# Kernel tuning notes

Measured on AMD Instinct MI355X. Metric: run time of the kernel, lower is better.

Reference implementation:

```python
import jax, jax.numpy as jnp
import numpy as np

NUM_HEADS = 16
HEAD_DIM = 64
D_DEC = 1024
D_ENC = 1024
R = 256  # kv_lora_rank
LN_EPS = 1e-5


def setup_inputs() -> dict:
    key = jax.random.key(0)
    ks = jax.random.split(key, 8)
    B, SQ, SK = 4, 2048, 4096
    query = jax.random.normal(ks[0], (B, SQ, D_DEC), dtype=jnp.float32)
    encoder_output = jax.random.normal(ks[1], (B, SK, D_ENC), dtype=jnp.float32)
    s = 0.02
    Wq = jax.random.normal(ks[2], (NUM_HEADS * HEAD_DIM, D_DEC), dtype=jnp.float32) * s
    Wkva = jax.random.normal(ks[3], (R, D_ENC), dtype=jnp.float32) * s
    ln_g = jnp.ones((R,), dtype=jnp.float32)
    ln_b = jnp.zeros((R,), dtype=jnp.float32)
    Wkvb = jax.random.normal(ks[4], (NUM_HEADS * 2 * HEAD_DIM, R), dtype=jnp.float32) * s
    Wout = jax.random.normal(ks[5], (D_DEC, NUM_HEADS * HEAD_DIM), dtype=jnp.float32) * s
    return {"query": query, "encoder_output": encoder_output, "Wq": Wq,
            "Wkva": Wkva, "ln_g": ln_g, "ln_b": ln_b, "Wkvb": Wkvb, "Wout": Wout}


def reference(query, encoder_output, Wq, Wkva, ln_g, ln_b, Wkvb, Wout):
    B, SQ, _ = query.shape
    SK = encoder_output.shape[1]
    H, Dh = NUM_HEADS, HEAD_DIM

    # q projection -> [B, H, SQ, Dh]
    q = jnp.einsum('bsd,ed->bse', query, Wq).reshape(B, SQ, H, Dh).transpose(0, 2, 1, 3)

    # low-rank KV compression + layernorm
    c = jnp.einsum('bsd,rd->bsr', encoder_output, Wkva)  # [B, SK, R]
    mu = jnp.mean(c, axis=-1, keepdims=True)
    var = jnp.mean(jnp.square(c - mu), axis=-1, keepdims=True)
    c = (c - mu) * jax.lax.rsqrt(var + LN_EPS) * ln_g + ln_b

    # decompress to K,V: [B, SK, H, 2*Dh] -> split
    kv = jnp.einsum('bsr,er->bse', c, Wkvb).reshape(B, SK, H, 2 * Dh).transpose(0, 2, 1, 3)
    k, v = kv[..., :Dh], kv[..., Dh:]

    scale = 1.0 / np.sqrt(Dh).astype(np.float32)
    scores = jnp.einsum('bhqd,bhkd->bhqk', q, k) * scale
    attn = jax.nn.softmax(scores, axis=-1)  # dropout is identity in eval / p=0
    o = jnp.einsum('bhqk,bhkd->bhqd', attn, v)
    o = o.transpose(0, 2, 1, 3).reshape(B, SQ, H * Dh)
    return jnp.einsum('bse,de->bsd', o, Wout)
```

## Files before the change

### kernel.cpp

```cpp
#include <hip/hip_runtime.h>

#define LOG2E 1.4426950408889634f

typedef __attribute__((ext_vector_type(8))) short short8;
typedef __attribute__((ext_vector_type(4))) float f32x4;
typedef __attribute__((ext_vector_type(16))) float f32x16;
typedef __attribute__((ext_vector_type(4))) unsigned u32x4;

__device__ inline unsigned short f2bf(float f) {
  unsigned u = __float_as_uint(f);
  u += 0x7fffu + ((u >> 16) & 1u);
  return (unsigned short)(u >> 16);
}

#define MFMA16(a, b, c) __builtin_amdgcn_mfma_f32_16x16x32_bf16((a), (b), (c), 0, 0, 0)
#define MFMA32(a, b, c) __builtin_amdgcn_mfma_f32_32x32x16_bf16((a), (b), (c), 0, 0, 0)

#define GLDS16(gp, lp)                                                              \
  __builtin_amdgcn_global_load_lds((const __attribute__((address_space(1))) void*)(gp), \
                                   (__attribute__((address_space(3))) void*)(lp), 16, 0, 0)

__device__ inline f32x4 zero4() {
  f32x4 z = {0.f, 0.f, 0.f, 0.f};
  return z;
}
__device__ inline f32x16 zero16() {
  f32x16 z = {0.f, 0.f, 0.f, 0.f, 0.f, 0.f, 0.f, 0.f, 0.f, 0.f, 0.f, 0.f, 0.f, 0.f, 0.f, 0.f};
  return z;
}
__device__ inline unsigned cvtpk_bf16(float a, float b) {
  unsigned r;
  asm("v_cvt_pk_bf16_f32 %0, %1, %2" : "=v"(r) : "v"(a), "v"(b));
  return r;
}
__device__ inline void plswap(unsigned& a, unsigned& b) {
  asm("v_permlane32_swap_b32 %0, %1" : "+v"(a), "+v"(b));
}

__global__ __launch_bounds__(256) void k_cast5(
    const float* __restrict__ q, const float* __restrict__ wq, const float* __restrict__ wo,
    const float* __restrict__ wb, const float* __restrict__ wa,
    unsigned short* __restrict__ qo, unsigned short* __restrict__ wqo, unsigned short* __restrict__ woo,
    unsigned short* __restrict__ wbo, unsigned short* __restrict__ wao) {
  int i = (blockIdx.x * 256 + threadIdx.x) * 4;
  const float* src;
  unsigned short* dst;
  int off;
  if (i < 8388608) { src = q; dst = qo; off = i; }
  else if (i < 9437184) { src = wq; dst = wqo; off = i - 8388608; }
  else if (i < 10485760) { src = wo; dst = woo; off = i - 9437184; }
  else if (i < 11010048) { src = wb; dst = wbo; off = i - 10485760; }
  else { src = wa; dst = wao; off = i - 11010048; }
  float4 v = *(const float4*)(src + off);
  unsigned lo = (unsigned)f2bf(v.x) | ((unsigned)f2bf(v.y) << 16);
  unsigned hi = (unsigned)f2bf(v.z) | ((unsigned)f2bf(v.w) << 16);
  *(uint2*)(dst + off) = make_uint2(lo, hi);
}

__global__ __launch_bounds__(256, 2) void k_qproj(const unsigned short* __restrict__ A,
                                                  const unsigned short* __restrict__ Bw,
                                                  unsigned short* __restrict__ Qout) {
  __shared__ __align__(16) short As[128 * 32];
  __shared__ __align__(16) short Bs[128 * 32];
  const int K = 1024;
  int tid = threadIdx.x;
  int w = tid >> 6, lane = tid & 63, quad = lane >> 4, c = lane & 15;
  int m0 = blockIdx.x * 128, n0 = blockIdx.y * 128;
  int wm = (w >> 1) * 64, wn = (w & 1) * 64;
  f32x4 acc[4][4];
#pragma unroll
  for (int i = 0; i < 4; i++)
#pragma unroll
    for (int j = 0; j < 4; j++) acc[i][j] = zero4();

  for (int k0 = 0; k0 < K; k0 += 32) {
#pragma unroll
    for (int i = 0; i < 2; i++) {
      int seg = w * 2 + i;
      int bo = seg * 1024 + lane * 16;
      int row = bo >> 6, col = (bo & 63) >> 1;
      GLDS16(A + (size_t)(m0 + row) * K + k0 + col, (char*)As + seg * 1024);
      GLDS16(Bw + (size_t)(n0 + row) * K + k0 + col, (char*)Bs + seg * 1024);
    }
    __syncthreads();
    short8 af[4], bfr[4];
#pragma unroll
    for (int i = 0; i < 4; i++) {
      af[i] = *(const short8*)&As[(wm + i * 16 + c) * 32 + quad * 8];
      bfr[i] = *(const short8*)&Bs[(wn + i * 16 + c) * 32 + quad * 8];
    }
#pragma unroll
    for (int mi = 0; mi < 4; mi++)
#pragma unroll
      for (int ni = 0; ni < 4; ni++) acc[mi][ni] = MFMA16(af[mi], bfr[ni], acc[mi][ni]);
    __syncthreads();
  }
  const float scale = 0.125f * LOG2E;
#pragma unroll
  for (int mi = 0; mi < 4; mi++) {
    int rowb = m0 + wm + mi * 16 + quad * 4;
#pragma unroll
    for (int ni = 0; ni < 4; ni++) {
      int col = n0 + wn + ni * 16 + c;
      int h = col >> 6, d = col & 63;
#pragma unroll
      for (int r = 0; r < 4; r++) {
        int row = rowb + r;
        int b = row >> 11, sq = row & 2047;
        Qout[(((size_t)(b * 16 + h)) * 2048 + sq) * 64 + d] = f2bf(acc[mi][ni][r] * scale);
      }
    }
  }
}

__global__ __launch_bounds__(256, 2) void k_cln(const float* __restrict__ E,
                                                const unsigned short* __restrict__ Wa,
                                                const float* __restrict__ g, const float* __restrict__ bb,
                                                unsigned short* __restrict__ Cout) {
  __shared__ __align__(16) short As[64 * 32];
  __shared__ __align__(16) short Bs[256 * 32];
  __shared__ float redS[4][64], redQ[4][64];
  __shared__ float gS[256], bS[256];
  const int K = 1024;
  int tid = threadIdx.x;
  int w = tid >> 6, lane = tid & 63, quad = lane >> 4, c = lane & 15;
  int m0 = blockIdx.x * 64;
  int rsub = lane >> 2, csub = (lane & 3) * 8;
  gS[tid] = g[tid];
  bS[tid] = bb[tid];
  f32x4 acc[4][4];
#pragma unroll
  for (int i = 0; i < 4; i++)
#pragma unroll
    for (int j = 0; j < 4; j++) acc[i][j] = zero4();

  for (int k0 = 0; k0 < K; k0 += 32) {
    {
      const float* Ep = E + (size_t)(m0 + w * 16 + rsub) * K + k0 + csub;
      float4 va = *(const float4*)Ep;
      float4 vb2 = *(const float4*)(Ep + 4);
      u32x4 pk = {cvtpk_bf16(va.x, va.y), cvtpk_bf16(va.z, va.w),
                  cvtpk_bf16(vb2.x, vb2.y), cvtpk_bf16(vb2.z, vb2.w)};
      *(u32x4*)((char*)As + w * 1024 + lane * 16) = pk;
    }
#pragma unroll
    for (int i = 0; i < 4; i++) {
      int seg = w * 4 + i;
      int bo = seg * 1024 + lane * 16;
      int row = bo >> 6, col = (bo & 63) >> 1;
      GLDS16(Wa + (size_t)row * K + k0 + col, (char*)Bs + seg * 1024);
    }
    __syncthreads();
    short8 af[4], bfr[4];
#pragma unroll
    for (int i = 0; i < 4; i++) {
      af[i] = *(const short8*)&As[(i * 16 + c) * 32 + quad * 8];
      bfr[i] = *(const short8*)&Bs[(w * 64 + i * 16 + c) * 32 + quad * 8];
    }
#pragma unroll
    for (int mi = 0; mi < 4; mi++)
#pragma unroll
      for (int ni = 0; ni < 4; ni++) acc[mi][ni] = MFMA16(af[mi], bfr[ni], acc[mi][ni]);
    __syncthreads();
  }
  float ps[4][4], pq[4][4];
#pragma unroll
  for (int mi = 0; mi < 4; mi++)
#pragma unroll
    for (int r = 0; r < 4; r++) {
      float s = 0.f, q = 0.f;
#pragma unroll
      for (int ni = 0; ni < 4; ni++) {
        float x = acc[mi][ni][r];
        s += x;
        q += x * x;
      }
      for (int m = 1; m < 16; m <<= 1) {
        s += __shfl_xor(s, m, 64);
        q += __shfl_xor(q, m, 64);
      }
      ps[mi][r] = s;
      pq[mi][r] = q;
    }
  if (c == 0) {
#pragma unroll
    for (int mi = 0; mi < 4; mi++)
#pragma unroll
      for (int r = 0; r < 4; r++) {
        int row = mi * 16 + quad * 4 + r;
        redS[w][row] = ps[mi][r];
        redQ[w][row] = pq[mi][r];
      }
  }
  __syncthreads();
  float muv[4][4], rsv[4][4];
#pragma unroll
  for (int mi = 0; mi < 4; mi++)
#pragma unroll
    for (int r = 0; r < 4; r++) {
      int row = mi * 16 + quad * 4 + r;
      float S = redS[0][row] + redS[1][row] + redS[2][row] + redS[3][row];
      float Q = redQ[0][row] + redQ[1][row] + redQ[2][row] + redQ[3][row];
      float mu = S * (1.f / 256.f);
      float var = Q * (1.f / 256.f) - mu * mu;
      muv[mi][r] = mu;
      rsv[mi][r] = rsqrtf(var + 1e-5f);
    }
#pragma unroll
  for (int mi = 0; mi < 4; mi++)
#pragma unroll
    for (int ni = 0; ni < 4; ni++) {
      int col = w * 64 + ni * 16 + c;
#pragma unroll
      for (int r = 0; r < 4; r++) {
        int row = m0 + mi * 16 + quad * 4 + r;
        float y = (acc[mi][ni][r] - muv[mi][r]) * rsv[mi][r] * gS[col] + bS[col];
        Cout[(size_t)row * 256 + col] = f2bf(y);
      }
    }
}

__global__ __launch_bounds__(256, 2) void k_kv(const unsigned short* __restrict__ A,
                                               const unsigned short* __restrict__ Bw,
                                               unsigned short* __restrict__ Kb,
                                               unsigned short* __restrict__ Vb) {
  __shared__ __align__(16) short As[128 * 32];
  __shared__ __align__(16) short Bs[128 * 32];
  const int K = 256;
  int tid = threadIdx.x;
  int w = tid >> 6, lane = tid & 63, quad = lane >> 4, c = lane & 15;
  int m0 = blockIdx.x * 128, n0 = blockIdx.y * 128;
  int wm = (w >> 1) * 64, wn = (w & 1) * 64;
  f32x4 acc[4][4];
#pragma unroll
  for (int i = 0; i < 4; i++)
#pragma unroll
    for (int j = 0; j < 4; j++) acc[i][j] = zero4();

  for (int k0 = 0; k0 < K; k0 += 32) {
#pragma unroll
    for (int i = 0; i < 2; i++) {
      int seg = w * 2 + i;
      int bo = seg * 1024 + lane * 16;
      int row = bo >> 6, col = (bo & 63) >> 1;
      GLDS16(A + (size_t)(m0 + row) * K + k0 + col, (char*)As + seg * 1024);
      GLDS16(Bw + (size_t)(n0 + row) * K + k0 + col, (char*)Bs + seg * 1024);
    }
    __syncthreads();
    short8 af[4], bfr[4];
#pragma unroll
    for (int i = 0; i < 4; i++) {
      af[i] = *(const short8*)&As[(wm + i * 16 + c) * 32 + quad * 8];
      bfr[i] = *(const short8*)&Bs[(wn + i * 16 + c) * 32 + quad * 8];
    }
#pragma unroll
    for (int mi = 0; mi < 4; mi++)
#pragma unroll
      for (int ni = 0; ni < 4; ni++) acc[mi][ni] = MFMA16(af[mi], bfr[ni], acc[mi][ni]);
    __syncthreads();
  }
#pragma unroll
  for (int mi = 0; mi < 4; mi++) {
    int rowb = m0 + wm + mi * 16 + quad * 4;
    int b = rowb >> 12;
    int sk0 = rowb & 4095;
    int kt = sk0 >> 6, ki0 = sk0 & 63;
    int sg = ((wm + mi * 16) & 63) >> 4;
    int khi = quad >> 1;
    int j0 = (quad & 1) * 4;
#pragma unroll
    for (int ni = 0; ni < 4; ni++) {
      int col = n0 + wn + ni * 16 + c;
      int h = col >> 7, rr = col & 127;
      size_t base = ((size_t)(b * 16 + h)) * 262144 + (size_t)kt * 4096;
      if (rr < 64) {
        int d = rr;
        int ds = d >> 4, dhi = (d >> 3) & 1, j = d & 7;
#pragma unroll
        for (int r = 0; r < 4; r++) {
          int ki = ki0 + r;
          int half = ki >> 5, l31k = ki & 31;
          Kb[base + (size_t)((half * 4 + ds) * 64 + l31k + 32 * dhi) * 8 + j] = f2bf(acc[mi][ni][r]);
        }
      } else {
        int d = rr - 64;
        int dt = d >> 5;
        unsigned lo = (unsigned)f2bf(acc[mi][ni][0]) | ((unsigned)f2bf(acc[mi][ni][1]) << 16);
        unsigned hi = (unsigned)f2bf(acc[mi][ni][2]) | ((unsigned)f2bf(acc[mi][ni][3]) << 16);
        *(uint2*)(Vb + base + (size_t)((dt * 4 + sg) * 64 + (d & 31) + 32 * khi) * 8 + j0) =
            make_uint2(lo, hi);
      }
    }
  }
}

__device__ __forceinline__ void attn_tile(const char* Kl, const char* Vl,
                                          const short8 (&qf)[4], f32x16 (&O)[2], float& lp) {
#pragma unroll
  for (int h = 0; h < 2; h++) {
    short8 kf[4];
#pragma unroll
    for (int ds = 0; ds < 4; ds++) kf[ds] = *(const short8*)(Kl + (h * 4 + ds) * 1024);
    f32x16 S = zero16();
#pragma unroll
    for (int ds = 0; ds < 4; ds++) S = MFMA32(kf[ds], qf[ds], S);
    float lpa = 0.f, lpb = 0.f;
    unsigned u[8];
#pragma unroll
    for (int m = 0; m < 8; m++) {
      float p0 = __builtin_amdgcn_exp2f(S[2 * m]);
      float p1 = __builtin_amdgcn_exp2f(S[2 * m + 1]);
      if (m & 1) lpb += p0 + p1; else lpa += p0 + p1;
      u[m] = cvtpk_bf16(p0, p1);
    }
    lp += lpa + lpb;
    plswap(u[0], u[2]);
    plswap(u[1], u[3]);
    plswap(u[4], u[6]);
    plswap(u[5], u[7]);
    u32x4 w0 = {u[0], u[1], u[2], u[3]};
    u32x4 w1 = {u[4], u[5], u[6], u[7]};
    short8 paf0 = __builtin_bit_cast(short8, w0);
    short8 paf1 = __builtin_bit_cast(short8, w1);
#pragma unroll
    for (int dt = 0; dt < 2; dt++) {
      short8 vf0 = *(const short8*)(Vl + (dt * 4 + h * 2 + 0) * 1024);
      short8 vf1 = *(const short8*)(Vl + (dt * 4 + h * 2 + 1) * 1024);
      O[dt] = MFMA32(paf0, vf0, O[dt]);
      O[dt] = MFMA32(paf1, vf1, O[dt]);
    }
  }
}

__global__ __launch_bounds__(256, 4) void k_attn(const unsigned short* __restrict__ Qb,
                                                 const unsigned short* __restrict__ Kb,
                                                 const unsigned short* __restrict__ Vb,
                                                 unsigned short* __restrict__ Ob) {
  __shared__ __align__(16) short KA[8192];
  __shared__ __align__(16) short KB[8192];
  int tid = threadIdx.x;
  int w = tid >> 6, lane = tid & 63;
  int l31 = lane & 31, hi = lane >> 5;
  int qt = blockIdx.x, bh = blockIdx.y;

  const char* Kg = (const char*)Kb + (size_t)bh * 524288;
  const char* Vg = (const char*)Vb + (size_t)bh * 524288;
  int ldsseg = (w < 2) ? w * 4 : 8 + (w - 2) * 4;
  const char* sgbase = ((w < 2) ? Kg + (w * 4) * 1024 : Vg + ((w - 2) * 4) * 1024) + lane * 16;

  const unsigned short* Qrow = Qb + ((size_t)bh * 2048 + qt * 128 + w * 32 + l31) * 64 + hi * 8;
  short8 qf[4];
#pragma unroll
  for (int ds = 0; ds < 4; ds++) qf[ds] = *(const short8*)(Qrow + ds * 16);

  f32x16 O[2];
  float lp = 0.f;
#pragma unroll
  for (int j = 0; j < 2; j++) O[j] = zero16();

#pragma unroll
  for (int i = 0; i < 4; i++) GLDS16(sgbase + i * 1024, (char*)KA + (ldsseg + i) * 1024);
  sgbase += 8192;
  __syncthreads();

  for (int kt2 = 0; kt2 < 64; kt2 += 2) {
    {
#pragma unroll
      for (int i = 0; i < 4; i++)
        GLDS16(sgbase + i * 1024, (char*)KB + (ldsseg + i) * 1024);
      sgbase += 8192;
      attn_tile((const char*)KA + lane * 16, (const char*)KA + lane * 16 + 8192, qf, O, lp);
      __syncthreads();
    }
    {
      if (kt2 < 62) {
#pragma unroll
        for (int i = 0; i < 4; i++)
          GLDS16(sgbase + i * 1024, (char*)KA + (ldsseg + i) * 1024);
        sgbase += 8192;
      }
      attn_tile((const char*)KB + lane * 16, (const char*)KB + lane * 16 + 8192, qf, O, lp);
      __syncthreads();
    }
  }

  lp += __shfl_xor(lp, 32, 64);
  int b = bh >> 4, hh = bh & 15;
#pragma unroll
  for (int r = 0; r < 16; r++) {
    int qrow = (r & 3) + 8 * (r >> 2) + 4 * hi;
    float inv = __builtin_amdgcn_rcpf(__shfl(lp, qrow, 64));
    size_t orow = ((size_t)b * 2048 + qt * 128 + w * 32 + qrow) * 1024 + hh * 64 + l31;
    Ob[orow] = f2bf(O[0][r] * inv);
    Ob[orow + 32] = f2bf(O[1][r] * inv);
  }
}

__global__ __launch_bounds__(256, 2) void k_out(const unsigned short* __restrict__ A,
                                                const unsigned short* __restrict__ Bw,
                                                float* __restrict__ Out) {
  __shared__ __align__(16) short As[128 * 32];
  __shared__ __align__(16) short Bs[128 * 32];
  const int K = 1024;
  int tid = threadIdx.x;
  int w = tid >> 6, lane = tid & 63, quad = lane >> 4, c = lane & 15;
  int m0 = blockIdx.x * 128, n0 = blockIdx.y * 128;
  int wm = (w >> 1) * 64, wn = (w & 1) * 64;
  f32x4 acc[4][4];
#pragma unroll
  for (int i = 0; i < 4; i++)
#pragma unroll
    for (int j = 0; j < 4; j++) acc[i][j] = zero4();

  for (int k0 = 0; k0 < K; k0 += 32) {
#pragma unroll
    for (int i = 0; i < 2; i++) {
      int seg = w * 2 + i;
      int bo = seg * 1024 + lane * 16;
      int row = bo >> 6, col = (bo & 63) >> 1;
      GLDS16(A + (size_t)(m0 + row) * K + k0 + col, (char*)As + seg * 1024);
      GLDS16(Bw + (size_t)(n0 + row) * K + k0 + col, (char*)Bs + seg * 1024);
    }
    __syncthreads();
    short8 af[4], bfr[4];
#pragma unroll
    for (int i = 0; i < 4; i++) {
      af[i] = *(const short8*)&As[(wm + i * 16 + c) * 32 + quad * 8];
      bfr[i] = *(const short8*)&Bs[(wn + i * 16 + c) * 32 + quad * 8];
    }
#pragma unroll
    for (int mi = 0; mi < 4; mi++)
#pragma unroll
      for (int ni = 0; ni < 4; ni++) acc[mi][ni] = MFMA16(af[mi], bfr[ni], acc[mi][ni]);
    __syncthreads();
  }
#pragma unroll
  for (int mi = 0; mi < 4; mi++) {
    int rowb = m0 + wm + mi * 16 + quad * 4;
#pragma unroll
    for (int ni = 0; ni < 4; ni++) {
      int col = n0 + wn + ni * 16 + c;
#pragma unroll
      for (int r = 0; r < 4; r++) Out[(size_t)(rowb + r) * 1024 + col] = acc[mi][ni][r];
    }
  }
}

extern "C" void kernel_launch(void* const* d_in, const int* in_sizes, int n_in,
                              void* d_out, int out_size, void* d_ws, size_t ws_size,
                              hipStream_t stream) {
  const float* query = (const float*)d_in[0];
  const float* enc = (const float*)d_in[1];
  const float* Wq = (const float*)d_in[2];
  const float* Wkva = (const float*)d_in[3];
  const float* ln_g = (const float*)d_in[4];
  const float* ln_b = (const float*)d_in[5];
  const float* Wkvb = (const float*)d_in[6];
  const float* Wout = (const float*)d_in[7];
  if (ws_size < 81264640) return;

  char* ws = (char*)d_ws;
  unsigned short* wq_bf = (unsigned short*)(ws + 0);
  unsigned short* wa_bf = (unsigned short*)(ws + 2097152);
  unsigned short* wb_bf = (unsigned short*)(ws + 2621440);
  unsigned short* wo_bf = (unsigned short*)(ws + 3670016);
  unsigned short* qproj = (unsigned short*)(ws + 5767168);
  unsigned short* cln = (unsigned short*)(ws + 22544384);
  unsigned short* vbuf = (unsigned short*)(ws + 30932992);
  unsigned short* qin_o = (unsigned short*)(ws + 64487424);
  unsigned short* kbuf = (unsigned short*)d_out;

  k_cast5<<<11008, 256, 0, stream>>>(query, Wq, Wout, Wkvb, Wkva,
                                     qin_o, wq_bf, wo_bf, wb_bf, wa_bf);

  k_qproj<<<dim3(64, 8), 256, 0, stream>>>(qin_o, wq_bf, qproj);
  k_cln<<<256, 256, 0, stream>>>(enc, wa_bf, ln_g, ln_b, cln);
  k_kv<<<dim3(128, 16), 256, 0, stream>>>(cln, wb_bf, kbuf, vbuf);
  k_attn<<<dim3(16, 64), 256, 0, stream>>>(qproj, kbuf, vbuf, qin_o);
  k_out<<<dim3(64, 8), 256, 0, stream>>>(qin_o, wo_bf, (float*)d_out);
}
```

Measured before the change: 405.9 us.

## Merge q-projection and KV-compression GEMMs into one launch; reorder attention grid

Combines the independent q-projection GEMM (512 tiles) and the compressed-KV GEMM with layernorm (256 tiles) into a single kernel of 768 blocks. Each group of three blocks handles two q tiles and one cln tile, using a shared LDS pool. This removes one launch and lets the two small, tail-heavy GEMMs fill the GPU together. The attention grid is also swapped so batch-head varies fastest across consecutive blocks, which changes L2 locality of the K/V reads. The merged kernel uses the larger LDS footprint for every block, which may reduce occupancy for the q-projection path.

```diff
diff --git a/kernel.cpp b/kernel.cpp
--- a/kernel.cpp
+++ b/kernel.cpp
@@ -57,167 +57,172 @@
   *(uint2*)(dst + off) = make_uint2(lo, hi);
 }
 
-__global__ __launch_bounds__(256, 2) void k_qproj(const unsigned short* __restrict__ A,
-                                                  const unsigned short* __restrict__ Bw,
-                                                  unsigned short* __restrict__ Qout) {
-  __shared__ __align__(16) short As[128 * 32];
-  __shared__ __align__(16) short Bs[128 * 32];
-  const int K = 1024;
+__global__ __launch_bounds__(256, 2) void k_qc(
+    const unsigned short* __restrict__ A, const unsigned short* __restrict__ Bw,
+    unsigned short* __restrict__ Qout,
+    const float* __restrict__ E, const unsigned short* __restrict__ Wa,
+    const float* __restrict__ g, const float* __restrict__ bb,
+    unsigned short* __restrict__ Cout) {
+  __shared__ __align__(16) char pool[24576];
+  int bx = blockIdx.x;
+  int grp = bx / 3, rem = bx - grp * 3;
   int tid = threadIdx.x;
   int w = tid >> 6, lane = tid & 63, quad = lane >> 4, c = lane & 15;
-  int m0 = blockIdx.x * 128, n0 = blockIdx.y * 128;
-  int wm = (w >> 1) * 64, wn = (w & 1) * 64;
-  f32x4 acc[4][4];
-#pragma unroll
-  for (int i = 0; i < 4; i++)
-#pragma unroll
-    for (int j = 0; j < 4; j++) acc[i][j] = zero4();
-
-  for (int k0 = 0; k0 < K; k0 += 32) {
-#pragma unroll
-    for (int i = 0; i < 2; i++) {
-      int seg = w * 2 + i;
-      int bo = seg * 1024 + lane * 16;
-      int row = bo >> 6, col = (bo & 63) >> 1;
-      GLDS16(A + (size_t)(m0 + row) * K + k0 + col, (char*)As + seg * 1024);
-      GLDS16(Bw + (size_t)(n0 + row) * K + k0 + col, (char*)Bs + seg * 1024);
+
+  if (rem < 2) {
+    short* As = (short*)pool;
+    short* Bs = (short*)(pool + 8192);
+    int qi = grp * 2 + rem;
+    const int K = 1024;
+    int m0 = (qi >> 3) * 128, n0 = (qi & 7) * 128;
+    int wm = (w >> 1) * 64, wn = (w & 1) * 64;
+    f32x4 acc[4][4];
+#pragma unroll
+    for (int i = 0; i < 4; i++)
+#pragma unroll
+      for (int j = 0; j < 4; j++) acc[i][j] = zero4();
+
+    for (int k0 = 0; k0 < K; k0 += 32) {
+#pragma unroll
+      for (int i = 0; i < 2; i++) {
+        int seg = w * 2 + i;
+        int bo = seg * 1024 + lane * 16;
+        int row = bo >> 6, col = (bo & 63) >> 1;
+        GLDS16(A + (size_t)(m0 + row) * K + k0 + col, (char*)As + seg * 1024);
+        GLDS16(Bw + (size_t)(n0 + row) * K + k0 + col, (char*)Bs + seg * 1024);
+      }
+      __syncthreads();
+      short8 af[4], bfr[4];
+#pragma unroll
+      for (int i = 0; i < 4; i++) {
+        af[i] = *(const short8*)&As[(wm + i * 16 + c) * 32 + quad * 8];
+        bfr[i] = *(const short8*)&Bs[(wn + i * 16 + c) * 32 + quad * 8];
+      }
+#pragma unroll
+      for (int mi = 0; mi < 4; mi++)
+#pragma unroll
+        for (int ni = 0; ni < 4; ni++) acc[mi][ni] = MFMA16(af[mi], bfr[ni], acc[mi][ni]);
+      __syncthreads();
+    }
+    const float scale = 0.125f * LOG2E;
+#pragma unroll
+    for (int mi = 0; mi < 4; mi++) {
+      int rowb = m0 + wm + mi * 16 + quad * 4;
+#pragma unroll
+      for (int ni = 0; ni < 4; ni++) {
+        int col = n0 + wn + ni * 16 + c;
+        int h = col >> 6, d = col & 63;
+#pragma unroll
+        for (int r = 0; r < 4; r++) {
+          int row = rowb + r;
+          int b = row >> 11, sq = row & 2047;
+          Qout[(((size_t)(b * 16 + h)) * 2048 + sq) * 64 + d] = f2bf(acc[mi][ni][r] * scale);
+        }
+      }
+    }
+  } else {
+    short* As = (short*)pool;
+    short* Bs = (short*)(pool + 4096);
+    float(*redS)[64] = (float(*)[64])(pool + 20480);
+    float(*redQ)[64] = (float(*)[64])(pool + 21504);
+    float* gS = (float*)(pool + 22528);
+    float* bS = (float*)(pool + 23552);
+    const int K = 1024;
+    int m0 = grp * 64;
+    int rsub = lane >> 2, csub = (lane & 3) * 8;
+    gS[tid] = g[tid];
+    bS[tid] = bb[tid];
+    f32x4 acc[4][4];
+#pragma unroll
+    for (int i = 0; i < 4; i++)
+#pragma unroll
+      for (int j = 0; j < 4; j++) acc[i][j] = zero4();
+
+    for (int k0 = 0; k0 < K; k0 += 32) {
+      {
+        const float* Ep = E + (size_t)(m0 + w * 16 + rsub) * K + k0 + csub;
+        float4 va = *(const float4*)Ep;
+        float4 vb2 = *(const float4*)(Ep + 4);
+        u32x4 pk = {cvtpk_bf16(va.x, va.y), cvtpk_bf16(va.z, va.w),
+                    cvtpk_bf16(vb2.x, vb2.y), cvtpk_bf16(vb2.z, vb2.w)};
+        *(u32x4*)((char*)As + w * 1024 + lane * 16) = pk;
+      }
+#pragma unroll
+      for (int i = 0; i < 4; i++) {
+        int seg = w * 4 + i;
+        int bo = seg * 1024 + lane * 16;
+        int row = bo >> 6, col = (bo & 63) >> 1;
+        GLDS16(Wa + (size_t)row * K + k0 + col, (char*)Bs + seg * 1024);
+      }
+      __syncthreads();
+      short8 af[4], bfr[4];
+#pragma unroll
+      for (int i = 0; i < 4; i++) {
+        af[i] = *(const short8*)&As[(i * 16 + c) * 32 + quad * 8];
+        bfr[i] = *(const short8*)&Bs[(w * 64 + i * 16 + c) * 32 + quad * 8];
+      }
+#pragma unroll
+      for (int mi = 0; mi < 4; mi++)
+#pragma unroll
+        for (int ni = 0; ni < 4; ni++) acc[mi][ni] = MFMA16(af[mi], bfr[ni], acc[mi][ni]);
+      __syncthreads();
+    }
+    float ps[4][4], pq[4][4];
+#pragma unroll
+    for (int mi = 0; mi < 4; mi++)
+#pragma unroll
+      for (int r = 0; r < 4; r++) {
+        float s = 0.f, q = 0.f;
+#pragma unroll
+        for (int ni = 0; ni < 4; ni++) {
+          float x = acc[mi][ni][r];
+          s += x;
+          q += x * x;
+        }
+        for (int m = 1; m < 16; m <<= 1) {
+          s += __shfl_xor(s, m, 64);
+          q += __shfl_xor(q, m, 64);
+        }
+        ps[mi][r] = s;
+        pq[mi][r] = q;
+      }
+    if (c == 0) {
+#pragma unroll
+      for (int mi = 0; mi < 4; mi++)
+#pragma unroll
+        for (int r = 0; r < 4; r++) {
+          int row = mi * 16 + quad * 4 + r;
+          redS[w][row] = ps[mi][r];
+          redQ[w][row] = pq[mi][r];
+        }
     }
     __syncthreads();
-    short8 af[4], bfr[4];
-#pragma unroll
-    for (int i = 0; i < 4; i++) {
-      af[i] = *(const short8*)&As[(wm + i * 16 + c) * 32 + quad * 8];
-      bfr[i] = *(const short8*)&Bs[(wn + i * 16 + c) * 32 + quad * 8];
-    }
-#pragma unroll
-    for (int mi = 0; mi < 4; mi++)
-#pragma unroll
-      for (int ni = 0; ni < 4; ni++) acc[mi][ni] = MFMA16(af[mi], bfr[ni], acc[mi][ni]);
-    __syncthreads();
-  }
-  const float scale = 0.125f * LOG2E;
-#pragma unroll
-  for (int mi = 0; mi < 4; mi++) {
-    int rowb = m0 + wm + mi * 16 + quad * 4;
-#pragma unroll
-    for (int ni = 0; ni < 4; ni++) {
-      int col = n0 + wn + ni * 16 + c;
-      int h = col >> 6, d = col & 63;
-#pragma unroll
-      for (int r = 0; r < 4; r++) {
-        int row = rowb + r;
-        int b = row >> 11, sq = row & 2047;
-        Qout[(((size_t)(b * 16 + h)) * 2048 + sq) * 64 + d] = f2bf(acc[mi][ni][r] * scale);
-      }
-    }
-  }
-}
-
-__global__ __launch_bounds__(256, 2) void k_cln(const float* __restrict__ E,
-                                                const unsigned short* __restrict__ Wa,
-                                                const float* __restrict__ g, const float* __restrict__ bb,
-                                                unsigned short* __restrict__ Cout) {
-  __shared__ __align__(16) short As[64 * 32];
-  __shared__ __align__(16) short Bs[256 * 32];
-  __shared__ float redS[4][64], redQ[4][64];
-  __shared__ float gS[256], bS[256];
-  const int K = 1024;
-  int tid = threadIdx.x;
-  int w = tid >> 6, lane = tid & 63, quad = lane >> 4, c = lane & 15;
-  int m0 = blockIdx.x * 64;
-  int rsub = lane >> 2, csub = (lane & 3) * 8;
-  gS[tid] = g[tid];
-  bS[tid] = bb[tid];
-  f32x4 acc[4][4];
-#pragma unroll
-  for (int i = 0; i < 4; i++)
-#pragma unroll
-    for (int j = 0; j < 4; j++) acc[i][j] = zero4();
-
-  for (int k0 = 0; k0 < K; k0 += 32) {
-    {
-      const float* Ep = E + (size_t)(m0 + w * 16 + rsub) * K + k0 + csub;
-      float4 va = *(const float4*)Ep;
-      float4 vb2 = *(const float4*)(Ep + 4);
-      u32x4 pk = {cvtpk_bf16(va.x, va.y), cvtpk_bf16(va.z, va.w),
-                  cvtpk_bf16(vb2.x, vb2.y), cvtpk_bf16(vb2.z, vb2.w)};
-      *(u32x4*)((char*)As + w * 1024 + lane * 16) = pk;
-    }
-#pragma unroll
-    for (int i = 0; i < 4; i++) {
-      int seg = w * 4 + i;
-      int bo = seg * 1024 + lane * 16;
-      int row = bo >> 6, col = (bo & 63) >> 1;
-      GLDS16(Wa + (size_t)row * K + k0 + col, (char*)Bs + seg * 1024);
-    }
-    __syncthreads();
-    short8 af[4], bfr[4];
-#pragma unroll
-    for (int i = 0; i < 4; i++) {
-      af[i] = *(const short8*)&As[(i * 16 + c) * 32 + quad * 8];
-      bfr[i] = *(const short8*)&Bs[(w * 64 + i * 16 + c) * 32 + quad * 8];
-    }
-#pragma unroll
-    for (int mi = 0; mi < 4; mi++)
-#pragma unroll
-      for (int ni = 0; ni < 4; ni++) acc[mi][ni] = MFMA16(af[mi], bfr[ni], acc[mi][ni]);
-    __syncthreads();
-  }
-  float ps[4][4], pq[4][4];
-#pragma unroll
-  for (int mi = 0; mi < 4; mi++)
-#pragma unroll
-    for (int r = 0; r < 4; r++) {
-      float s = 0.f, q = 0.f;
-#pragma unroll
-      for (int ni = 0; ni < 4; ni++) {
-        float x = acc[mi][ni][r];
-        s += x;
-        q += x * x;
-      }
-      for (int m = 1; m < 16; m <<= 1) {
-        s += __shfl_xor(s, m, 64);
-        q += __shfl_xor(q, m, 64);
-      }
-      ps[mi][r] = s;
-      pq[mi][r] = q;
-    }
-  if (c == 0) {
+    float muv[4][4], rsv[4][4];
 #pragma unroll
     for (int mi = 0; mi < 4; mi++)
 #pragma unroll
       for (int r = 0; r < 4; r++) {
         int row = mi * 16 + quad * 4 + r;
-        redS[w][row] = ps[mi][r];
-        redQ[w][row] = pq[mi][r];
-      }
-  }
-  __syncthreads();
-  float muv[4][4], rsv[4][4];
-#pragma unroll
-  for (int mi = 0; mi < 4; mi++)
-#pragma unroll
-    for (int r = 0; r < 4; r++) {
-      int row = mi * 16 + quad * 4 + r;
-      float S = redS[0][row] + redS[1][row] + redS[2][row] + redS[3][row];
-      float Q = redQ[0][row] + redQ[1][row] + redQ[2][row] + redQ[3][row];
-      float mu = S * (1.f / 256.f);
-      float var = Q * (1.f / 256.f) - mu * mu;
-      muv[mi][r] = mu;
-      rsv[mi][r] = rsqrtf(var + 1e-5f);
-    }
-#pragma unroll
-  for (int mi = 0; mi < 4; mi++)
-#pragma unroll
-    for (int ni = 0; ni < 4; ni++) {
-      int col = w * 64 + ni * 16 + c;
-#pragma unroll
-      for (int r = 0; r < 4; r++) {
-        int row = m0 + mi * 16 + quad * 4 + r;
-        float y = (acc[mi][ni][r] - muv[mi][r]) * rsv[mi][r] * gS[col] + bS[col];
-        Cout[(size_t)row * 256 + col] = f2bf(y);
-      }
-    }
+        float S = redS[0][row] + redS[1][row] + redS[2][row] + redS[3][row];
+        float Q = redQ[0][row] + redQ[1][row] + redQ[2][row] + redQ[3][row];
+        float mu = S * (1.f / 256.f);
+        float var = Q * (1.f / 256.f) - mu * mu;
+        muv[mi][r] = mu;
+        rsv[mi][r] = rsqrtf(var + 1e-5f);
+      }
+#pragma unroll
+    for (int mi = 0; mi < 4; mi++)
+#pragma unroll
+      for (int ni = 0; ni < 4; ni++) {
+        int col = w * 64 + ni * 16 + c;
+#pragma unroll
+        for (int r = 0; r < 4; r++) {
+          int row = m0 + mi * 16 + quad * 4 + r;
+          float y = (acc[mi][ni][r] - muv[mi][r]) * rsv[mi][r] * gS[col] + bS[col];
+          Cout[(size_t)row * 256 + col] = f2bf(y);
+        }
+      }
+  }
 }
 
 __global__ __launch_bounds__(256, 2) void k_kv(const unsigned short* __restrict__ A,
@@ -341,7 +346,7 @@
   int tid = threadIdx.x;
   int w = tid >> 6, lane = tid & 63;
   int l31 = lane & 31, hi = lane >> 5;
-  int qt = blockIdx.x, bh = blockIdx.y;
+  int bh = blockIdx.x, qt = blockIdx.y;
 
   const char* Kg = (const char*)Kb + (size_t)bh * 524288;
   const char* Vg = (const char*)Vb + (size_t)bh * 524288;
@@ -473,9 +478,8 @@
   k_cast5<<<11008, 256, 0, stream>>>(query, Wq, Wout, Wkvb, Wkva,
                                      qin_o, wq_bf, wo_bf, wb_bf, wa_bf);
 
-  k_qproj<<<dim3(64, 8), 256, 0, stream>>>(qin_o, wq_bf, qproj);
-  k_cln<<<256, 256, 0, stream>>>(enc, wa_bf, ln_g, ln_b, cln);
+  k_qc<<<768, 256, 0, stream>>>(qin_o, wq_bf, qproj, enc, wa_bf, ln_g, ln_b, cln);
   k_kv<<<dim3(128, 16), 256, 0, stream>>>(cln, wb_bf, kbuf, vbuf);
-  k_attn<<<dim3(16, 64), 256, 0, stream>>>(qproj, kbuf, vbuf, qin_o);
+  k_attn<<<dim3(64, 16), 256, 0, stream>>>(qproj, kbuf, vbuf, qin_o);
   k_out<<<dim3(64, 8), 256, 0, stream>>>(qin_o, wo_bf, (float*)d_out);
 }
```

Result: faster. 396.7 us (-2.3%).
